# Kernel tuning notes

Hardware: AMD Instinct MI355X
Metric: run time of the kernel (lower is better)

The kernel has to match this reference:

```python
import jax, jax.numpy as jnp
import numpy as np

D_MODEL = 768
D_FF = 3072
N_HEADS = 12
D_QUART = D_MODEL // 4  # 192
EPS = 1e-5


def layer_norm(x, g, b):
    mu = jnp.mean(x, axis=-1, keepdims=True)
    var = jnp.mean((x - mu) ** 2, axis=-1, keepdims=True)
    return (x - mu) * jax.lax.rsqrt(var + EPS) * g + b


def setup_inputs() -> dict:
    key = jax.random.key(0)
    ks = jax.random.split(key, 24)
    d, dff, dq = D_MODEL, D_FF, D_QUART
    s = lambda k, shape, fan: jax.random.normal(k, shape, jnp.float32) * (1.0 / np.sqrt(fan))
    return {
        "x": jax.random.normal(ks[0], (8, 1024, d), jnp.float32),
        # distance_proj: Linear(1, d//4) -> weight [dq], bias [dq]
        "dp_w": s(ks[1], (dq,), 1), "dp_b": jnp.zeros((dq,), jnp.float32),
        # spatial_encoding: Linear(d,d) GELU Linear(d,d)
        "se_w1": s(ks[2], (d, d), d), "se_b1": jnp.zeros((d,), jnp.float32),
        "se_w2": s(ks[3], (d, d), d), "se_b2": jnp.zeros((d,), jnp.float32),
        # attention projections (stored [in, out])
        "wq": s(ks[4], (d, d), d), "bq": jnp.zeros((d,), jnp.float32),
        "wk": s(ks[5], (d, d), d), "bk": jnp.zeros((d,), jnp.float32),
        "wv": s(ks[6], (d, d), d), "bv": jnp.zeros((d,), jnp.float32),
        "wo": s(ks[7], (d, d), d), "bo": jnp.zeros((d,), jnp.float32),
        # geometric_net FFN
        "gw1": s(ks[8], (d, dff), d), "gb1": jnp.zeros((dff,), jnp.float32),
        "gw2": s(ks[9], (dff, d), dff), "gb2": jnp.zeros((d,), jnp.float32),
        # layer norms
        "n1_g": jnp.ones((d,), jnp.float32), "n1_b": jnp.zeros((d,), jnp.float32),
        "n2_g": jnp.ones((d,), jnp.float32), "n2_b": jnp.zeros((d,), jnp.float32),
    }


def _forward(x, dp_w, dp_b, se_w1, se_b1, se_w2, se_b2,
             wq, bq, wk, bk, wv, bv, wo, bo,
             gw1, gb1, gw2, gb2, n1_g, n1_b, n2_g, n2_b):
    B, N, d = x.shape
    # --- compute_spatial_features ---
    # ||x_i - x_j|| via Gram trick (avoids [B,N,N,d] intermediate)
    sq = jnp.sum(x * x, axis=-1)                      # [B,N]
    gram = jnp.einsum('bnd,bmd->bnm', x, x)           # [B,N,N]
    d2 = jnp.maximum(sq[:, :, None] + sq[:, None, :] - 2.0 * gram, 0.0)
    dist = jnp.sqrt(d2)                               # [B,N,N]
    # Linear(1, d/4) then mean over j commutes: project the mean distance
    mean_d = jnp.mean(dist, axis=2)                   # [B,N]
    spat = mean_d[..., None] * dp_w + dp_b            # [B,N,d/4]
    spat = jnp.pad(spat, ((0, 0), (0, 0), (0, d - D_QUART)))  # [B,N,d]
    # spatial_encoding MLP (exact GELU, matching torch nn.GELU default)
    h = jax.nn.gelu(spat @ se_w1 + se_b1, approximate=False)
    x = x + (h @ se_w2 + se_b2)
    # --- attention block ---
    res = x
    xn = layer_norm(x, n1_g, n1_b)
    H, dh = N_HEADS, d // N_HEADS
    q = (xn @ wq + bq).reshape(B, N, H, dh)
    k = (xn @ wk + bk).reshape(B, N, H, dh)
    v = (xn @ wv + bv).reshape(B, N, H, dh)
    scores = jnp.einsum('bqhd,bkhd->bhqk', q, k) / np.sqrt(dh)
    attn = jax.nn.softmax(scores, axis=-1)
    o = jnp.einsum('bhqk,bkhd->bqhd', attn, v).reshape(B, N, d)
    x = res + (o @ wo + bo)
    # --- FFN block ---
    res = x
    xn = layer_norm(x, n2_g, n2_b)
    h = jax.nn.gelu(xn @ gw1 + gb1, approximate=False)
    x = res + (h @ gw2 + gb2)
    return x


def reference(x, dp_w, dp_b, se_w1, se_b1, se_w2, se_b2,
              wq, bq, wk, bk, wv, bv, wo, bo,
              gw1, gb1, gw2, gb2, n1_g, n1_b, n2_g, n2_b):
    return _forward(x, dp_w, dp_b, se_w1, se_b1, se_w2, se_b2,
                    wq, bq, wk, bk, wv, bv, wo, bo,
                    gw1, gb1, gw2, gb2, n1_g, n1_b, n2_g, n2_b)
```

## Files before the change

kernel.cpp:

```cpp
#include <hip/hip_runtime.h>
#include <hip/hip_bf16.h>

typedef unsigned short ushort;
typedef __attribute__((ext_vector_type(8))) __bf16 bf16x8;
typedef __attribute__((ext_vector_type(4))) float f32x4;
typedef __attribute__((ext_vector_type(8))) ushort ushort8;

__device__ inline ushort f2bf(float f) {
    union { float f; unsigned u; } a{f};
    unsigned r = a.u + 0x7FFFu + ((a.u >> 16) & 1u);
    return (ushort)(r >> 16);
}
__device__ inline float gelu_f(float x) {
    return 0.5f * x * (1.f + erff(x * 0.70710678118654752f));
}

__global__ void prep_all(const float* __restrict__ se_w2, ushort* __restrict__ sw2t,
                         const float* __restrict__ wq, ushort* __restrict__ wqt,
                         const float* __restrict__ wk, ushort* __restrict__ wkt,
                         const float* __restrict__ wv, ushort* __restrict__ wvt,
                         const float* __restrict__ wo, ushort* __restrict__ wot,
                         const float* __restrict__ gw1, ushort* __restrict__ g1t,
                         const float* __restrict__ gw2, ushort* __restrict__ g2t,
                         const float* __restrict__ x, ushort* __restrict__ xb,
                         float* __restrict__ sq,
                         const float* __restrict__ bq, const float* __restrict__ bk,
                         const float* __restrict__ bv, float* __restrict__ bqkv,
                         float* __restrict__ meanv,
                         const float* __restrict__ dp_w, const float* __restrict__ dp_b,
                         const float* __restrict__ se_w1, const float* __restrict__ se_b1,
                         float* __restrict__ Avec, float* __restrict__ Cvec) {
    __shared__ float tile[32][33];
    __shared__ float wsum[4];
    int bid = blockIdx.x;
    int tid = threadIdx.x;
    if (bid < 7488) {
        const float* Wm; ushort* Wt; int K, N, kx, ny;
        if (bid < 2880) {
            int task = bid / 576, tt = bid % 576;
            kx = tt % 24; ny = tt / 24; K = 768; N = 768;
            switch (task) {
                case 0: Wm = se_w2; Wt = sw2t; break;
                case 1: Wm = wq; Wt = wqt; break;
                case 2: Wm = wk; Wt = wkt; break;
                case 3: Wm = wv; Wt = wvt; break;
                default: Wm = wo; Wt = wot; break;
            }
        } else if (bid < 5184) {
            int tt = bid - 2880; kx = tt % 24; ny = tt / 24; K = 768; N = 3072;
            Wm = gw1; Wt = g1t;
        } else {
            int tt = bid - 5184; kx = tt % 96; ny = tt / 96; K = 3072; N = 768;
            Wm = gw2; Wt = g2t;
        }
        int k0 = kx * 32, n0 = ny * 32;
        int tx = tid & 31, ty = tid >> 5;
        #pragma unroll
        for (int r = ty; r < 32; r += 8) tile[r][tx] = Wm[(size_t)(k0 + r) * N + n0 + tx];
        __syncthreads();
        #pragma unroll
        for (int r = ty; r < 32; r += 8) Wt[(size_t)(n0 + r) * K + k0 + tx] = f2bf(tile[tx][r]);
    } else if (bid < 15680) {
        int row = bid - 7488;
        const float* xr = x + (size_t)row * 768;
        ushort* xbr = xb + (size_t)row * 768;
        float s = 0.f;
        #pragma unroll
        for (int i = 0; i < 3; ++i) {
            float vv = xr[tid + i * 256];
            xbr[tid + i * 256] = f2bf(vv);
            s += vv * vv;
        }
        #pragma unroll
        for (int off = 1; off < 64; off <<= 1) s += __shfl_xor(s, off);
        if ((tid & 63) == 0) wsum[tid >> 6] = s;
        __syncthreads();
        if (tid == 0) sq[row] = wsum[0] + wsum[1] + wsum[2] + wsum[3];
    } else if (bid < 15683) {
        int o = (bid - 15680) * 256 + tid;
        float a = 0.f, c = 0.f;
        for (int i = 0; i < 192; ++i) {
            float w = se_w1[(size_t)i * 768 + o];
            a += dp_w[i] * w;
            c += dp_b[i] * w;
        }
        Avec[o] = a;
        Cvec[o] = c + se_b1[o];
    } else if (bid < 15715) {
        meanv[(bid - 15683) * 256 + tid] = 0.f;
    } else {
        for (int i = tid; i < 2304; i += 256) {
            float v = (i < 768) ? bq[i] : (i < 1536 ? bk[i - 768] : bv[i - 1536]);
            bqkv[i] = v;
        }
    }
}

__global__ void hgen(const float* __restrict__ mean_acc, const float* __restrict__ Avec,
                     const float* __restrict__ Cvec, ushort* __restrict__ h) {
    int row = blockIdx.x;
    float md = mean_acc[row] * (1.f / 1024.f);
    int t = threadIdx.x;
    #pragma unroll
    for (int i = 0; i < 3; ++i) {
        int o = t + i * 256;
        h[(size_t)row * 768 + o] = f2bf(gelu_f(md * Avec[o] + Cvec[o]));
    }
}

__global__ void lnorm(const float* __restrict__ xin, const float* __restrict__ g,
                      const float* __restrict__ b, ushort* __restrict__ xn) {
    int row = blockIdx.x;
    const float* xr = xin + (size_t)row * 768;
    int t = threadIdx.x;
    float v[3];
    float s = 0.f, s2 = 0.f;
    #pragma unroll
    for (int i = 0; i < 3; ++i) {
        v[i] = xr[t + i * 256];
        s += v[i];
        s2 += v[i] * v[i];
    }
    #pragma unroll
    for (int off = 1; off < 64; off <<= 1) { s += __shfl_xor(s, off); s2 += __shfl_xor(s2, off); }
    __shared__ float a0[4], a1[4];
    if ((t & 63) == 0) { a0[t >> 6] = s; a1[t >> 6] = s2; }
    __syncthreads();
    s = a0[0] + a0[1] + a0[2] + a0[3];
    s2 = a1[0] + a1[1] + a1[2] + a1[3];
    float mu = s * (1.f / 768.f);
    float var = s2 * (1.f / 768.f) - mu * mu;
    float rs = rsqrtf(var + 1e-5f);
    #pragma unroll
    for (int i = 0; i < 3; ++i) {
        int o = t + i * 256;
        xn[(size_t)row * 768 + o] = f2bf((v[i] - mu) * rs * g[o] + b[o]);
    }
}

#define BM 128
#define BK 32

enum { EPI_BF16 = 0, EPI_GELU = 1, EPI_RES = 2, EPI_GRAM = 3, EPI_QKV = 4, EPI_RESK = 5 };

template <int EPI, int BNT>
__launch_bounds__(256, BNT == 64 ? 4 : 2)
__global__ void gemm_bt(const ushort* __restrict__ A, const ushort* __restrict__ Bt,
                        int M, int N, int K,
                        const float* __restrict__ bias,
                        const float* res, float* outf,
                        ushort* __restrict__ outh,
                        const float* __restrict__ sq, float* __restrict__ mean_acc) {
    __shared__ __align__(16) ushort As[2][BM * BK];
    __shared__ __align__(16) ushort Bs[2][BNT * BK];

    unsigned gx = gridDim.x, gy = gridDim.y;
    unsigned flat = blockIdx.x + gx * (blockIdx.y + gy * blockIdx.z);
    unsigned total = gx * gy * gridDim.z;
    unsigned chunk = total >> 3;
    flat = (flat & 7) * chunk + (flat >> 3);
    unsigned bx = flat % gx;
    unsigned rem = flat / gx;
    unsigned by = rem % gy;
    unsigned bz = rem / gy;

    int m0 = bx * BM;
    int n0 = by * BNT;
    if (EPI == EPI_GRAM) {
        A += (size_t)bz * 1024 * 768;
        Bt = A;
        sq += bz * 1024;
        mean_acc += bz * 1024;
    }
    int t = threadIdx.x, w = t >> 6, l = t & 63;
    int lg = l >> 4, li = l & 15;
    constexpr int MI = (BNT == 128) ? 4 : 2;
    int wm = (BNT == 128) ? (w >> 1) * 64 : w * 32;
    int wn = (BNT == 128) ? (w & 1) * 64 : 0;

    int srow = l >> 2, scol = (l & 3) * 8;
    const ushort* agp0 = A + (size_t)(m0 + (2 * w) * 16 + srow) * K + scol;
    const ushort* agp1 = A + (size_t)(m0 + (2 * w + 1) * 16 + srow) * K + scol;
    const ushort* bgp0;
    const ushort* bgp1 = nullptr;
    ushort* la0 = &As[0][(2 * w) * 16 * BK];
    ushort* lb0;
    if (BNT == 128) {
        bgp0 = Bt + (size_t)(n0 + (2 * w) * 16 + srow) * K + scol;
        bgp1 = Bt + (size_t)(n0 + (2 * w + 1) * 16 + srow) * K + scol;
        lb0 = &Bs[0][(2 * w) * 16 * BK];
    } else {
        bgp0 = Bt + (size_t)(n0 + w * 16 + srow) * K + scol;
        lb0 = &Bs[0][w * 16 * BK];
    }

    f32x4 acc[MI][4] = {};

    auto stage = [&](int buf, int kt) {
        size_t ko = (size_t)kt * BK;
        ushort* la = la0 + buf * (BM * BK);
        ushort* lb = lb0 + buf * (BNT * BK);
        __builtin_amdgcn_global_load_lds((const __attribute__((address_space(1))) void*)(agp0 + ko),
                                         (__attribute__((address_space(3))) void*)la, 16, 0, 0);
        __builtin_amdgcn_global_load_lds((const __attribute__((address_space(1))) void*)(agp1 + ko),
                                         (__attribute__((address_space(3))) void*)(la + 16 * BK), 16, 0, 0);
        __builtin_amdgcn_global_load_lds((const __attribute__((address_space(1))) void*)(bgp0 + ko),
                                         (__attribute__((address_space(3))) void*)lb, 16, 0, 0);
        if (BNT == 128)
            __builtin_amdgcn_global_load_lds((const __attribute__((address_space(1))) void*)(bgp1 + ko),
                                             (__attribute__((address_space(3))) void*)(lb + 16 * BK), 16, 0, 0);
    };

    int nk = K / BK;
    stage(0, 0);
    __syncthreads();
    int buf = 0;
    for (int kt = 0; kt < nk; ++kt) {
        if (kt + 1 < nk) stage(buf ^ 1, kt + 1);
        bf16x8 af[MI], bfr[4];
        #pragma unroll
        for (int i = 0; i < MI; ++i)
            af[i] = *reinterpret_cast<const bf16x8*>(&As[buf][(wm + i * 16 + li) * BK + lg * 8]);
        #pragma unroll
        for (int i = 0; i < 4; ++i)
            bfr[i] = *reinterpret_cast<const bf16x8*>(&Bs[buf][(wn + i * 16 + li) * BK + lg * 8]);
        #pragma unroll
        for (int mi = 0; mi < MI; ++mi)
            #pragma unroll
            for (int ni = 0; ni < 4; ++ni)
                acc[mi][ni] = __builtin_amdgcn_mfma_f32_16x16x32_bf16(af[mi], bfr[ni], acc[mi][ni], 0, 0, 0);
        __syncthreads();
        buf ^= 1;
    }

    #pragma unroll
    for (int mi = 0; mi < MI; ++mi) {
        #pragma unroll
        for (int r = 0; r < 4; ++r) {
            int row = m0 + wm + mi * 16 + lg * 4 + r;
            if (EPI == EPI_GRAM) {
                float si = sq[row];
                float s = 0.f;
                #pragma unroll
                for (int ni = 0; ni < 4; ++ni) {
                    int col = n0 + wn + ni * 16 + li;
                    float d2 = si + sq[col] - 2.f * acc[mi][ni][r];
                    s += sqrtf(fmaxf(d2, 0.f));
                }
                s += __shfl_xor(s, 1); s += __shfl_xor(s, 2);
                s += __shfl_xor(s, 4); s += __shfl_xor(s, 8);
                if (li == 0) atomicAdd(&mean_acc[row], s);
            } else {
                #pragma unroll
                for (int ni = 0; ni < 4; ++ni) {
                    int col = n0 + wn + ni * 16 + li;
                    float v = acc[mi][ni][r] + bias[col];
                    if (EPI == EPI_BF16) outh[(size_t)row * N + col] = f2bf(v);
                    if (EPI == EPI_GELU) outh[(size_t)row * N + col] = f2bf(gelu_f(v));
                    if (EPI == EPI_RES) outf[(size_t)row * N + col] = res[(size_t)row * N + col] + v;
                    if (EPI == EPI_QKV) {
                        int which = col / 768;
                        int c2 = col - which * 768;
                        outh[(size_t)which * (8192 * 768) + (size_t)row * 768 + c2] = f2bf(v);
                    }
                }
            }
        }
    }
}

template <int EPI>
__launch_bounds__(256, 3)
__global__ void gemm4(const ushort* __restrict__ A, const ushort* __restrict__ Bt,
                      int M, int N, int K,
                      const float* __restrict__ bias,
                      const float* res, float* outf, ushort* __restrict__ outh) {
    __shared__ __align__(16) ushort As[3][128 * 32];
    __shared__ __align__(16) ushort Bs[3][128 * 32];

    unsigned gx = gridDim.x, gy = gridDim.y;
    unsigned orig = blockIdx.x + gx * (blockIdx.y + gy * blockIdx.z);
    unsigned xcd = orig & 7;
    unsigned q = orig >> 3;
    unsigned mpg = gx >> 3;
    unsigned mloc = q % mpg;
    unsigned rest = q / mpg;
    unsigned n = rest % gy;
    unsigned split = rest / gy;
    int m0 = (xcd * mpg + mloc) * 128;
    int n0 = n * 128;
    int Keff = (EPI == EPI_RESK) ? (K >> 1) : K;
    int kbase = (EPI == EPI_RESK) ? (int)split * Keff : 0;

    int t = threadIdx.x, w = t >> 6, l = t & 63;
    int lg = l >> 4, li = l & 15;
    int wm = (w >> 1) * 64, wn = (w & 1) * 64;

    int srow = l >> 2;
    int scol = ((l & 3) ^ ((l >> 3) & 3)) * 8;
    const ushort* agp0 = A + (size_t)(m0 + (2 * w) * 16 + srow) * K + kbase + scol;
    const ushort* agp1 = A + (size_t)(m0 + (2 * w + 1) * 16 + srow) * K + kbase + scol;
    const ushort* bgp0 = Bt + (size_t)(n0 + (2 * w) * 16 + srow) * K + kbase + scol;
    const ushort* bgp1 = Bt + (size_t)(n0 + (2 * w + 1) * 16 + srow) * K + kbase + scol;

    f32x4 acc[4][4] = {};

    auto stage = [&](int buf, int kt) {
        size_t ko = (size_t)kt * 32;
        ushort* la = &As[buf][(2 * w) * 16 * 32];
        ushort* lb = &Bs[buf][(2 * w) * 16 * 32];
        __builtin_amdgcn_global_load_lds((const __attribute__((address_space(1))) void*)(agp0 + ko),
                                         (__attribute__((address_space(3))) void*)la, 16, 0, 0);
        __builtin_amdgcn_global_load_lds((const __attribute__((address_space(1))) void*)(agp1 + ko),
                                         (__attribute__((address_space(3))) void*)(la + 16 * 32), 16, 0, 0);
        __builtin_amdgcn_global_load_lds((const __attribute__((address_space(1))) void*)(bgp0 + ko),
                                         (__attribute__((address_space(3))) void*)lb, 16, 0, 0);
        __builtin_amdgcn_global_load_lds((const __attribute__((address_space(1))) void*)(bgp1 + ko),
                                         (__attribute__((address_space(3))) void*)(lb + 16 * 32), 16, 0, 0);
    };

    int nk = Keff / 32;
    stage(0, 0);
    stage(1, 1);
    int rdsw = (lg ^ ((li >> 1) & 3)) * 8;
    for (int kt = 0; kt < nk; ++kt) {
        int buf = kt % 3;
        if (kt + 1 < nk) asm volatile("s_waitcnt vmcnt(4)" ::: "memory");
        else             asm volatile("s_waitcnt vmcnt(0)" ::: "memory");
        asm volatile("s_barrier" ::: "memory");
        __builtin_amdgcn_sched_barrier(0);
        bf16x8 af[4], bfr[4];
        #pragma unroll
        for (int i = 0; i < 4; ++i) {
            af[i] = *reinterpret_cast<const bf16x8*>(&As[buf][(wm + i * 16 + li) * 32 + rdsw]);
            bfr[i] = *reinterpret_cast<const bf16x8*>(&Bs[buf][(wn + i * 16 + li) * 32 + rdsw]);
        }
        __builtin_amdgcn_s_setprio(1);
        #pragma unroll
        for (int mi = 0; mi < 4; ++mi)
            #pragma unroll
            for (int ni = 0; ni < 4; ++ni)
                acc[mi][ni] = __builtin_amdgcn_mfma_f32_16x16x32_bf16(af[mi], bfr[ni], acc[mi][ni], 0, 0, 0);
        __builtin_amdgcn_s_setprio(0);
        if (kt + 2 < nk) stage((kt + 2) % 3, kt + 2);
    }

    #pragma unroll
    for (int mi = 0; mi < 4; ++mi) {
        #pragma unroll
        for (int r = 0; r < 4; ++r) {
            int row = m0 + wm + mi * 16 + lg * 4 + r;
            #pragma unroll
            for (int ni = 0; ni < 4; ++ni) {
                int col = n0 + wn + ni * 16 + li;
                if (EPI == EPI_RESK) {
                    float v = acc[mi][ni][r] + (split == 0 ? bias[col] : 0.f);
                    atomicAdd(&outf[(size_t)row * N + col], v);
                } else {
                    float v = acc[mi][ni][r] + bias[col];
                    if (EPI == EPI_GELU) outh[(size_t)row * N + col] = f2bf(gelu_f(v));
                    if (EPI == EPI_RES)  outf[(size_t)row * N + col] = res[(size_t)row * N + col] + v;
                    if (EPI == EPI_QKV) {
                        int which = col / 768;
                        int c2 = col - which * 768;
                        outh[(size_t)which * (8192 * 768) + (size_t)row * 768 + c2] = f2bf(v);
                    }
                }
            }
        }
    }
}

__launch_bounds__(256, 3)
__global__ void flash_attn(const ushort* __restrict__ q, const ushort* __restrict__ k,
                           const ushort* __restrict__ v, ushort* __restrict__ o) {
    int flat = blockIdx.x + 8 * (blockIdx.y + 12 * blockIdx.z);
    flat = (flat & 7) * 96 + (flat >> 3);
    int qt = flat & 7;
    int rem = flat >> 3;
    int h = rem % 12;
    int b = rem / 12;

    int t = threadIdx.x, w = t >> 6, l = t & 63;
    int lg = l >> 4, li = l & 15;

    __shared__ __align__(16) ushort Vt[2][64][72];
    __shared__ __align__(16) ushort P[4][32][72];
    __shared__ __align__(16) ushort Ks[2][64 * 64];

    const size_t hoff = (size_t)h * 64;
    const size_t bbase = (size_t)b * 1024 * 768;
    const ushort* kbase = &k[bbase + hoff];

    bf16x8 qf[2][2];
    #pragma unroll
    for (int f = 0; f < 2; ++f) {
        int qrow = qt * 128 + w * 32 + f * 16 + li;
        const ushort* qp = &q[bbase + (size_t)qrow * 768 + hoff];
        qf[f][0] = *reinterpret_cast<const bf16x8*>(qp + lg * 8);
        qf[f][1] = *reinterpret_cast<const bf16x8*>(qp + 32 + lg * 8);
    }

    bf16x8 onesf;
    #pragma unroll
    for (int i = 0; i < 8; ++i) onesf[i] = (__bf16)1.0f;

    float m_[2][4];
    f32x4 oacc[2][4];
    f32x4 oell[2];
    #pragma unroll
    for (int f = 0; f < 2; ++f) {
        #pragma unroll
        for (int r = 0; r < 4; ++r) m_[f][r] = -1e30f;
        oell[f] = f32x4{0.f, 0.f, 0.f, 0.f};
        #pragma unroll
        for (int n = 0; n < 4; ++n) oacc[f][n] = f32x4{0.f, 0.f, 0.f, 0.f};
    }

    int vrow = t & 63;
    int vc = t >> 6;
    const ushort* vbase = &v[bbase + hoff];

    auto stageK = [&](int kbuf, int jtile) {
        #pragma unroll
        for (int j = 0; j < 2; ++j) {
            int c = (w * 2 + j) * 64 + l;
            int krow = c >> 3, kcc = c & 7;
            int srcc = (kcc & 4) | ((kcc & 3) ^ (krow & 3));
            const ushort* src = &kbase[(size_t)(jtile * 64 + krow) * 768 + srcc * 8];
            __builtin_amdgcn_global_load_lds(
                (const __attribute__((address_space(1))) void*)src,
                (__attribute__((address_space(3))) void*)&Ks[kbuf][c * 8], 16, 0, 0);
        }
    };

    stageK(0, 0);
    ushort8 vv0 = *reinterpret_cast<const ushort8*>(&vbase[(size_t)vrow * 768 + vc * 8]);
    ushort8 vv1 = *reinterpret_cast<const ushort8*>(&vbase[(size_t)vrow * 768 + (vc + 4) * 8]);
    __syncthreads();

    int kch = lg ^ (li & 3);

    for (int jt = 0; jt < 16; ++jt) {
        int j0 = jt * 64, buf = jt & 1;
        #pragma unroll
        for (int i = 0; i < 8; ++i) Vt[buf][vc * 8 + i][vrow] = vv0[i];
        #pragma unroll
        for (int i = 0; i < 8; ++i) Vt[buf][(vc + 4) * 8 + i][vrow] = vv1[i];
        if (jt < 15) {
            vv0 = *reinterpret_cast<const ushort8*>(&vbase[(size_t)(j0 + 64 + vrow) * 768 + vc * 8]);
            vv1 = *reinterpret_cast<const ushort8*>(&vbase[(size_t)(j0 + 64 + vrow) * 768 + (vc + 4) * 8]);
            stageK(buf ^ 1, jt + 1);
        }
        f32x4 s[2][4];
        __builtin_amdgcn_s_setprio(1);
        #pragma unroll
        for (int jj = 0; jj < 4; ++jj) {
            int krow = jj * 16 + li;
            bf16x8 kf0 = *reinterpret_cast<const bf16x8*>(&Ks[buf][krow * 64 + kch * 8]);
            bf16x8 kf1 = *reinterpret_cast<const bf16x8*>(&Ks[buf][krow * 64 + 32 + kch * 8]);
            #pragma unroll
            for (int f = 0; f < 2; ++f) {
                f32x4 a = {0.f, 0.f, 0.f, 0.f};
                a = __builtin_amdgcn_mfma_f32_16x16x32_bf16(qf[f][0], kf0, a, 0, 0, 0);
                a = __builtin_amdgcn_mfma_f32_16x16x32_bf16(qf[f][1], kf1, a, 0, 0, 0);
                s[f][jj] = a * 0.125f;
            }
        }
        __builtin_amdgcn_s_setprio(0);
        #pragma unroll
        for (int f = 0; f < 2; ++f) {
            float mt[4];
            #pragma unroll
            for (int r = 0; r < 4; ++r)
                mt[r] = fmaxf(fmaxf(s[f][0][r], s[f][1][r]), fmaxf(s[f][2][r], s[f][3][r]));
            #pragma unroll
            for (int r = 0; r < 4; ++r) {
                mt[r] = fmaxf(mt[r], __shfl_xor(mt[r], 1));
                mt[r] = fmaxf(mt[r], __shfl_xor(mt[r], 2));
                mt[r] = fmaxf(mt[r], __shfl_xor(mt[r], 4));
                mt[r] = fmaxf(mt[r], __shfl_xor(mt[r], 8));
            }
            bool need = (mt[0] > m_[f][0] + 8.f) | (mt[1] > m_[f][1] + 8.f) |
                        (mt[2] > m_[f][2] + 8.f) | (mt[3] > m_[f][3] + 8.f);
            if (__any(need)) {
                #pragma unroll
                for (int r = 0; r < 4; ++r) {
                    float mn = fmaxf(m_[f][r], mt[r]);
                    float al = __expf(m_[f][r] - mn);
                    m_[f][r] = mn;
                    #pragma unroll
                    for (int n = 0; n < 4; ++n) oacc[f][n][r] *= al;
                    oell[f][r] *= al;
                }
            }
            #pragma unroll
            for (int jj = 0; jj < 4; ++jj)
                #pragma unroll
                for (int r = 0; r < 4; ++r)
                    P[w][f * 16 + lg * 4 + r][jj * 16 + li] = f2bf(__expf(s[f][jj][r] - m_[f][r]));
        }
        __syncthreads();
        bf16x8 pf[2][2];
        #pragma unroll
        for (int f = 0; f < 2; ++f) {
            pf[f][0] = *reinterpret_cast<const bf16x8*>(&P[w][f * 16 + li][lg * 8]);
            pf[f][1] = *reinterpret_cast<const bf16x8*>(&P[w][f * 16 + li][32 + lg * 8]);
        }
        __builtin_amdgcn_s_setprio(1);
        #pragma unroll
        for (int f = 0; f < 2; ++f) {
            oell[f] = __builtin_amdgcn_mfma_f32_16x16x32_bf16(pf[f][0], onesf, oell[f], 0, 0, 0);
            oell[f] = __builtin_amdgcn_mfma_f32_16x16x32_bf16(pf[f][1], onesf, oell[f], 0, 0, 0);
        }
        #pragma unroll
        for (int n = 0; n < 4; ++n) {
            bf16x8 vf0 = *reinterpret_cast<const bf16x8*>(&Vt[buf][n * 16 + li][lg * 8]);
            bf16x8 vf1 = *reinterpret_cast<const bf16x8*>(&Vt[buf][n * 16 + li][32 + lg * 8]);
            #pragma unroll
            for (int f = 0; f < 2; ++f) {
                oacc[f][n] = __builtin_amdgcn_mfma_f32_16x16x32_bf16(pf[f][0], vf0, oacc[f][n], 0, 0, 0);
                oacc[f][n] = __builtin_amdgcn_mfma_f32_16x16x32_bf16(pf[f][1], vf1, oacc[f][n], 0, 0, 0);
            }
        }
        __builtin_amdgcn_s_setprio(0);
    }
    #pragma unroll
    for (int f = 0; f < 2; ++f)
        #pragma unroll
        for (int n = 0; n < 4; ++n)
            #pragma unroll
            for (int r = 0; r < 4; ++r) {
                int row = qt * 128 + w * 32 + f * 16 + lg * 4 + r;
                o[bbase + (size_t)row * 768 + hoff + n * 16 + li] = f2bf(oacc[f][n][r] / oell[f][r]);
            }
}

extern "C" void kernel_launch(void* const* d_in, const int* in_sizes, int n_in,
                              void* d_out, int out_size, void* d_ws, size_t ws_size,
                              hipStream_t stream) {
    const float* x = (const float*)d_in[0];
    const float* dp_w = (const float*)d_in[1];
    const float* dp_b = (const float*)d_in[2];
    const float* se_w1 = (const float*)d_in[3];
    const float* se_b1 = (const float*)d_in[4];
    const float* se_w2 = (const float*)d_in[5];
    const float* se_b2 = (const float*)d_in[6];
    const float* wq = (const float*)d_in[7];  const float* bq = (const float*)d_in[8];
    const float* wk = (const float*)d_in[9];  const float* bk = (const float*)d_in[10];
    const float* wv = (const float*)d_in[11]; const float* bv = (const float*)d_in[12];
    const float* wo = (const float*)d_in[13]; const float* bo = (const float*)d_in[14];
    const float* gw1 = (const float*)d_in[15]; const float* gb1 = (const float*)d_in[16];
    const float* gw2 = (const float*)d_in[17]; const float* gb2 = (const float*)d_in[18];
    const float* n1g = (const float*)d_in[19]; const float* n1b = (const float*)d_in[20];
    const float* n2g = (const float*)d_in[21]; const float* n2b = (const float*)d_in[22];
    float* out = (float*)d_out;

    constexpr size_t SZ_ACT = (size_t)8192 * 768 * 2;
    char* W = (char*)d_ws;
    ushort* xb = (ushort*)(W);
    ushort* q_ = (ushort*)(W + SZ_ACT);
    ushort* k_ = (ushort*)(W + 2 * SZ_ACT);
    ushort* v_ = (ushort*)(W + 3 * SZ_ACT);
    ushort* o_ = (ushort*)(W + 4 * SZ_ACT);
    ushort* hsp = q_;
    ushort* hff = q_;
    ushort* wqt = (ushort*)(W + 5 * SZ_ACT);
    ushort* wkt = wqt + (size_t)768 * 768;
    ushort* wvt = wkt + (size_t)768 * 768;
    ushort* wot = wvt + (size_t)768 * 768;
    ushort* sw2t = wot + (size_t)768 * 768;
    ushort* g1t = sw2t + (size_t)768 * 768;
    ushort* g2t = g1t + (size_t)768 * 3072;
    float* sqv = (float*)(g2t + (size_t)3072 * 768);
    float* meanv = sqv + 8192;
    float* Avec = meanv + 8192;
    float* Cvec = Avec + 768;
    float* bqkv = Cvec + 768;

    prep_all<<<15716, 256, 0, stream>>>(se_w2, sw2t, wq, wqt, wk, wkt, wv, wvt,
                                        wo, wot, gw1, g1t, gw2, g2t,
                                        x, xb, sqv, bq, bk, bv, bqkv, meanv,
                                        dp_w, dp_b, se_w1, se_b1, Avec, Cvec);

    gemm_bt<EPI_GRAM, 128><<<dim3(8, 8, 8), 256, 0, stream>>>(xb, xb, 1024, 1024, 768,
                                                              nullptr, nullptr, nullptr, nullptr, sqv, meanv);
    hgen<<<8192, 256, 0, stream>>>(meanv, Avec, Cvec, hsp);
    gemm4<EPI_RES><<<dim3(64, 6), 256, 0, stream>>>(hsp, sw2t, 8192, 768, 768,
                                                    se_b2, x, out, nullptr);
    lnorm<<<8192, 256, 0, stream>>>(out, n1g, n1b, xb);
    gemm4<EPI_QKV><<<dim3(64, 18), 256, 0, stream>>>(xb, wqt, 8192, 2304, 768,
                                                     bqkv, nullptr, nullptr, q_);
    flash_attn<<<dim3(8, 12, 8), 256, 0, stream>>>(q_, k_, v_, o_);
    gemm4<EPI_RES><<<dim3(64, 6), 256, 0, stream>>>(o_, wot, 8192, 768, 768,
                                                    bo, out, out, nullptr);
    lnorm<<<8192, 256, 0, stream>>>(out, n2g, n2b, xb);
    gemm4<EPI_GELU><<<dim3(64, 24), 256, 0, stream>>>(xb, g1t, 8192, 3072, 768,
                                                      gb1, nullptr, nullptr, hff);
    gemm4<EPI_RESK><<<dim3(64, 6, 2), 256, 0, stream>>>(hff, g2t, 8192, 768, 3072,
                                                        gb2, nullptr, out, nullptr);
}
```

Baseline: 390.0 us.

## Replace split-K atomic FFN down-projection with 256x128 tile 8-wave GEMM

The FFN second GEMM (K=3072) used to run as split-K over two slices with fp32 atomicAdd into the output. It now runs as a new 512-thread kernel with 256x128 output tiles, BK=64, XOR-swizzled LDS, triple buffering, and a plain residual-add epilogue. This removes the atomics and the extra output traffic, but the grid shrinks to 192 blocks, which may underfill the GPU. Separately, flash attention folds log2(e) into the score scale and uses exp2f in place of __expf.

```diff
diff --git a/kernel.cpp b/kernel.cpp
--- a/kernel.cpp
+++ b/kernel.cpp
@@ -141,7 +141,7 @@
 #define BM 128
 #define BK 32
 
-enum { EPI_BF16 = 0, EPI_GELU = 1, EPI_RES = 2, EPI_GRAM = 3, EPI_QKV = 4, EPI_RESK = 5 };
+enum { EPI_BF16 = 0, EPI_GELU = 1, EPI_RES = 2, EPI_GRAM = 3, EPI_QKV = 4 };
 
 template <int EPI, int BNT>
 __launch_bounds__(256, BNT == 64 ? 4 : 2)
@@ -286,11 +286,8 @@
     unsigned mloc = q % mpg;
     unsigned rest = q / mpg;
     unsigned n = rest % gy;
-    unsigned split = rest / gy;
     int m0 = (xcd * mpg + mloc) * 128;
     int n0 = n * 128;
-    int Keff = (EPI == EPI_RESK) ? (K >> 1) : K;
-    int kbase = (EPI == EPI_RESK) ? (int)split * Keff : 0;
 
     int t = threadIdx.x, w = t >> 6, l = t & 63;
     int lg = l >> 4, li = l & 15;
@@ -298,10 +295,10 @@
 
     int srow = l >> 2;
     int scol = ((l & 3) ^ ((l >> 3) & 3)) * 8;
-    const ushort* agp0 = A + (size_t)(m0 + (2 * w) * 16 + srow) * K + kbase + scol;
-    const ushort* agp1 = A + (size_t)(m0 + (2 * w + 1) * 16 + srow) * K + kbase + scol;
-    const ushort* bgp0 = Bt + (size_t)(n0 + (2 * w) * 16 + srow) * K + kbase + scol;
-    const ushort* bgp1 = Bt + (size_t)(n0 + (2 * w + 1) * 16 + srow) * K + kbase + scol;
+    const ushort* agp0 = A + (size_t)(m0 + (2 * w) * 16 + srow) * K + scol;
+    const ushort* agp1 = A + (size_t)(m0 + (2 * w + 1) * 16 + srow) * K + scol;
+    const ushort* bgp0 = Bt + (size_t)(n0 + (2 * w) * 16 + srow) * K + scol;
+    const ushort* bgp1 = Bt + (size_t)(n0 + (2 * w + 1) * 16 + srow) * K + scol;
 
     f32x4 acc[4][4] = {};
 
@@ -319,7 +316,7 @@
                                          (__attribute__((address_space(3))) void*)(lb + 16 * 32), 16, 0, 0);
     };
 
-    int nk = Keff / 32;
+    int nk = K / 32;
     stage(0, 0);
     stage(1, 1);
     int rdsw = (lg ^ ((li >> 1) & 3)) * 8;
@@ -353,19 +350,120 @@
             #pragma unroll
             for (int ni = 0; ni < 4; ++ni) {
                 int col = n0 + wn + ni * 16 + li;
-                if (EPI == EPI_RESK) {
-                    float v = acc[mi][ni][r] + (split == 0 ? bias[col] : 0.f);
-                    atomicAdd(&outf[(size_t)row * N + col], v);
-                } else {
-                    float v = acc[mi][ni][r] + bias[col];
-                    if (EPI == EPI_GELU) outh[(size_t)row * N + col] = f2bf(gelu_f(v));
-                    if (EPI == EPI_RES)  outf[(size_t)row * N + col] = res[(size_t)row * N + col] + v;
-                    if (EPI == EPI_QKV) {
-                        int which = col / 768;
-                        int c2 = col - which * 768;
-                        outh[(size_t)which * (8192 * 768) + (size_t)row * 768 + c2] = f2bf(v);
-                    }
+                float v = acc[mi][ni][r] + bias[col];
+                if (EPI == EPI_GELU) outh[(size_t)row * N + col] = f2bf(gelu_f(v));
+                if (EPI == EPI_RES)  outf[(size_t)row * N + col] = res[(size_t)row * N + col] + v;
+                if (EPI == EPI_QKV) {
+                    int which = col / 768;
+                    int c2 = col - which * 768;
+                    outh[(size_t)which * (8192 * 768) + (size_t)row * 768 + c2] = f2bf(v);
                 }
+            }
+        }
+    }
+}
+
+template <int EPI>
+__launch_bounds__(512, 2)
+__global__ void gemm8(const ushort* __restrict__ A, const ushort* __restrict__ Bt,
+                      int M, int N, int K,
+                      const float* __restrict__ bias,
+                      const float* res, float* outf, ushort* __restrict__ outh) {
+    __shared__ __align__(16) ushort As[3][2][128 * 64];
+    __shared__ __align__(16) ushort Bs[3][2][64 * 64];
+
+    unsigned gx = gridDim.x;
+    unsigned orig = blockIdx.x + gx * blockIdx.y;
+    unsigned xcd = orig & 7;
+    unsigned q = orig >> 3;
+    unsigned mpg = gx >> 3;
+    unsigned mloc = q % mpg;
+    unsigned n = q / mpg;
+    int m0 = (xcd * mpg + mloc) * 256;
+    int n0 = n * 128;
+
+    int t = threadIdx.x, w = t >> 6, l = t & 63;
+    int lg = l >> 4, li = l & 15;
+    int wr = w >> 1, wc = w & 1;
+    int ha = wr >> 1;
+    int ra = (wr & 1) * 64;
+
+    f32x4 acc[4][4] = {};
+
+    auto stage = [&](int buf, int kt) {
+        int k0 = kt * 64;
+        #pragma unroll
+        for (int h = 0; h < 2; ++h) {
+            #pragma unroll
+            for (int jj = 0; jj < 2; ++jj) {
+                int d = (2 * w + jj) * 1024 + l * 16;
+                int dp = d ^ (((d >> 7) & 7) << 4);
+                const ushort* src = A + (size_t)(m0 + h * 128 + (dp >> 7)) * K + k0 + ((dp & 127) >> 1);
+                __builtin_amdgcn_global_load_lds(
+                    (const __attribute__((address_space(1))) void*)src,
+                    (__attribute__((address_space(3))) void*)&As[buf][h][(2 * w + jj) * 512], 16, 0, 0);
+            }
+            {
+                int d = w * 1024 + l * 16;
+                int dp = d ^ (((d >> 7) & 7) << 4);
+                const ushort* src = Bt + (size_t)(n0 + h * 64 + (dp >> 7)) * K + k0 + ((dp & 127) >> 1);
+                __builtin_amdgcn_global_load_lds(
+                    (const __attribute__((address_space(1))) void*)src,
+                    (__attribute__((address_space(3))) void*)&Bs[buf][h][w * 512], 16, 0, 0);
+            }
+        }
+    };
+
+    int nk = K / 64;
+    stage(0, 0);
+    stage(1, 1);
+    stage(2, 2);
+    for (int kt = 0; kt < nk; ++kt) {
+        int buf = kt % 3;
+        if (kt + 2 < nk)      asm volatile("s_waitcnt vmcnt(12)" ::: "memory");
+        else if (kt + 1 < nk) asm volatile("s_waitcnt vmcnt(6)" ::: "memory");
+        else                  asm volatile("s_waitcnt vmcnt(0)" ::: "memory");
+        asm volatile("s_barrier" ::: "memory");
+        __builtin_amdgcn_sched_barrier(0);
+        #pragma unroll
+        for (int kk = 0; kk < 2; ++kk) {
+            bf16x8 af[4], bf[4];
+            #pragma unroll
+            for (int mi = 0; mi < 4; ++mi) {
+                int e = (ra + mi * 16 + li) * 128 + kk * 64 + lg * 16;
+                int ep = e ^ (((e >> 7) & 7) << 4);
+                af[mi] = *reinterpret_cast<const bf16x8*>(&As[buf][ha][ep >> 1]);
+            }
+            #pragma unroll
+            for (int ni = 0; ni < 4; ++ni) {
+                int e = (ni * 16 + li) * 128 + kk * 64 + lg * 16;
+                int ep = e ^ (((e >> 7) & 7) << 4);
+                bf[ni] = *reinterpret_cast<const bf16x8*>(&Bs[buf][wc][ep >> 1]);
+            }
+            __builtin_amdgcn_s_setprio(1);
+            #pragma unroll
+            for (int mi = 0; mi < 4; ++mi)
+                #pragma unroll
+                for (int ni = 0; ni < 4; ++ni)
+                    acc[mi][ni] = __builtin_amdgcn_mfma_f32_16x16x32_bf16(af[mi], bf[ni], acc[mi][ni], 0, 0, 0);
+            __builtin_amdgcn_s_setprio(0);
+        }
+        asm volatile("s_barrier" ::: "memory");
+        __builtin_amdgcn_sched_barrier(0);
+        if (kt + 3 < nk) stage(buf, kt + 3);
+    }
+
+    #pragma unroll
+    for (int mi = 0; mi < 4; ++mi) {
+        #pragma unroll
+        for (int r = 0; r < 4; ++r) {
+            int row = m0 + wr * 64 + mi * 16 + lg * 4 + r;
+            #pragma unroll
+            for (int ni = 0; ni < 4; ++ni) {
+                int col = n0 + wc * 64 + ni * 16 + li;
+                float v = acc[mi][ni][r] + bias[col];
+                if (EPI == EPI_GELU) outh[(size_t)row * N + col] = f2bf(gelu_f(v));
+                if (EPI == EPI_RES)  outf[(size_t)row * N + col] = res[(size_t)row * N + col] + v;
             }
         }
     }
@@ -405,6 +503,9 @@
     #pragma unroll
     for (int i = 0; i < 8; ++i) onesf[i] = (__bf16)1.0f;
 
+    const float SSC = 0.125f * 1.44269504088896f;
+    const float THR = 8.f * 1.44269504088896f;
+
     float m_[2][4];
     f32x4 oacc[2][4];
     f32x4 oell[2];
@@ -464,7 +565,7 @@
                 f32x4 a = {0.f, 0.f, 0.f, 0.f};
                 a = __builtin_amdgcn_mfma_f32_16x16x32_bf16(qf[f][0], kf0, a, 0, 0, 0);
                 a = __builtin_amdgcn_mfma_f32_16x16x32_bf16(qf[f][1], kf1, a, 0, 0, 0);
-                s[f][jj] = a * 0.125f;
+                s[f][jj] = a * SSC;
             }
         }
         __builtin_amdgcn_s_setprio(0);
@@ -481,13 +582,13 @@
                 mt[r] = fmaxf(mt[r], __shfl_xor(mt[r], 4));
                 mt[r] = fmaxf(mt[r], __shfl_xor(mt[r], 8));
             }
-            bool need = (mt[0] > m_[f][0] + 8.f) | (mt[1] > m_[f][1] + 8.f) |
-                        (mt[2] > m_[f][2] + 8.f) | (mt[3] > m_[f][3] + 8.f);
+            bool need = (mt[0] > m_[f][0] + THR) | (mt[1] > m_[f][1] + THR) |
+                        (mt[2] > m_[f][2] + THR) | (mt[3] > m_[f][3] + THR);
             if (__any(need)) {
                 #pragma unroll
                 for (int r = 0; r < 4; ++r) {
                     float mn = fmaxf(m_[f][r], mt[r]);
-                    float al = __expf(m_[f][r] - mn);
+                    float al = exp2f(m_[f][r] - mn);
                     m_[f][r] = mn;
                     #pragma unroll
                     for (int n = 0; n < 4; ++n) oacc[f][n][r] *= al;
@@ -498,7 +599,7 @@
             for (int jj = 0; jj < 4; ++jj)
                 #pragma unroll
                 for (int r = 0; r < 4; ++r)
-                    P[w][f * 16 + lg * 4 + r][jj * 16 + li] = f2bf(__expf(s[f][jj][r] - m_[f][r]));
+                    P[w][f * 16 + lg * 4 + r][jj * 16 + li] = f2bf(exp2f(s[f][jj][r] - m_[f][r]));
         }
         __syncthreads();
         bf16x8 pf[2][2];
@@ -597,6 +698,6 @@
     lnorm<<<8192, 256, 0, stream>>>(out, n2g, n2b, xb);
     gemm4<EPI_GELU><<<dim3(64, 24), 256, 0, stream>>>(xb, g1t, 8192, 3072, 768,
                                                       gb1, nullptr, nullptr, hff);
-    gemm4<EPI_RESK><<<dim3(64, 6, 2), 256, 0, stream>>>(hff, g2t, 8192, 768, 3072,
-                                                        gb2, nullptr, out, nullptr);
-}
+    gemm8<EPI_RES><<<dim3(32, 6), 512, 0, stream>>>(hff, g2t, 8192, 768, 3072,
+                                                    gb2, out, out, nullptr);
+}
```

Measured after the change: 397.3 us. No clear change (+1.9%).
